# Kernel tuning notes

Measured on AMD Instinct MI355X. Metric: run time of the kernel, lower is better.

Reference implementation:

```python
import jax, jax.numpy as jnp
import numpy as np

CX, CY, FX, FY = 334.081, 169.808, 460.585, 460.268
EPS = 1e-07
T_ITER = 1000
MIN_POINTS = 5000
H, W, B = 360, 640, 2


def _point_cloud(depth_img):
    # depth_img: [C,H,W]; channel 2 if C==3 else channel 0
    depth = depth_img[2] if depth_img.shape[0] == 3 else depth_img[0]
    rows, cols = depth.shape
    c = jnp.arange(cols, dtype=depth.dtype)[None, :]
    r = jnp.arange(rows, dtype=depth.dtype)[:, None]
    valid = (depth > 0) & (depth < 65535)
    nanv = jnp.float32(jnp.nan)
    z = jnp.where(valid, depth / 1000.0, nanv)
    x = jnp.where(valid, z * (c - CX) / FX, nanv)
    y = jnp.where(valid, z * (r - CY) / FY, nanv)
    pcd = jnp.stack([x.ravel(), y.ravel(), z.ravel()], axis=1)  # [N,3]
    return pcd, valid.ravel()


def setup_inputs() -> dict:
    key = jax.random.key(0)
    k1, k2 = jax.random.split(key)
    fake = jax.random.uniform(k1, (B, 1, H, W), dtype=jnp.float32)
    real = jax.random.uniform(k2, (B, 1, H, W), dtype=jnp.float32)
    return {"fake": fake, "real": real, "epoch": 5, "show_image": 0}


def _forward(fake, real, epoch):
    real_pcd, vr = _point_cloud(real[0])
    fake_pcd, vf = _point_cloud(fake[0])
    real_pcd = real_pcd * 1000.0
    fake_pcd = fake_pcd * 1000.0
    # pcd[pcd==0] = eps  (NaN==0 is False, NaNs preserved)
    real_pcd = jnp.where(real_pcd == 0, EPS, real_pcd)
    fake_pcd = jnp.where(fake_pcd == 0, EPS, fake_pcd)

    # combined validity mask (real-valid then fake-valid filtering chain)
    m = vr & vf
    cnt = jnp.maximum(jnp.sum(m), 1)

    def sel(v, fill):
        return jnp.where(m, v, fill)

    def mrmse(a, b):
        d = sel(a, 0.0) - sel(b, 0.0)
        return jnp.sqrt(jnp.sum(d * d) / cnt)

    lossX = mrmse(real_pcd[:, 0], fake_pcd[:, 0])
    lossY = mrmse(real_pcd[:, 1], fake_pcd[:, 1])
    lossZ = mrmse(real_pcd[:, 2], fake_pcd[:, 2])
    dlog = jnp.log(jnp.abs(sel(real_pcd[:, 2], 1.0))) - jnp.log(jnp.abs(sel(fake_pcd[:, 2], 1.0)))
    RMSE_log = 10000.0 * jnp.sqrt(jnp.sum(jnp.where(m, dlog * dlog, 0.0)) / cnt)
    loss17 = RMSE_log * jnp.abs(10.0 * (3.0 - jnp.exp(lossX) - jnp.exp(lossY) - jnp.exp(lossZ)))

    # ---- batched RANSAC plane fit on normalized fake cloud ----
    nan_cloud = jnp.where(jnp.isnan(fake_pcd), 0.0, fake_pcd)
    pts = nan_cloud / jnp.max(nan_cloud)  # [N,3]
    N = pts.shape[0]
    thresh = jnp.maximum(jnp.float32(0.025 - 0.001 * epoch), jnp.float32(0.005))

    rkey = jax.random.key(42)
    idx = jax.random.randint(rkey, (T_ITER, 3), 0, N)  # 3 sample points per trial
    p = pts[idx]  # [T,3,3]
    vA = p[:, 1] - p[:, 0]
    vB = p[:, 2] - p[:, 0]
    nrm = jnp.cross(vA, vB)
    nrm = nrm / jnp.linalg.norm(nrm, axis=1, keepdims=True)  # unit normals [T,3]
    kk = -jnp.sum(nrm * p[:, 1], axis=1)  # plane offsets [T]
    dist = pts @ nrm.T + kk[None, :]  # [N,T], |n|=1 so no extra divide
    inl = jnp.abs(dist) <= thresh  # [N,T]
    counts = jnp.sum(inl, axis=0)  # [T]
    # keep first trial with strictly-largest count among counts > minPoints
    score = jnp.where(counts > MIN_POINTS, counts, -1)
    best = jnp.argmax(score)
    a, b, c, d = nrm[best, 0], nrm[best, 1], nrm[best, 2], kk[best]
    inlier_mask = inl[:, best]  # [N]

    # translation/rotation were built via torch.tensor(...) -> detached in torch
    trans = jax.lax.stop_gradient(jnp.stack([jnp.zeros(()), jnp.zeros(()), d / c]))
    n2 = a * a + b * b + c * c
    cos_t = c / jnp.sqrt(n2)
    sin_t = jnp.sqrt((a * a + b * b) / n2)
    sab = jnp.sqrt(a * a + b * b)
    u1 = b / sab
    u2 = -a / sab
    R = jnp.stack([
        jnp.stack([cos_t + u1 * u1 * (1 - cos_t), u1 * u2 * (1 - cos_t), u2 * sin_t]),
        jnp.stack([u1 * u2 * (1 - cos_t), cos_t + u2 * u2 * (1 - cos_t), -u1 * sin_t]),
        jnp.stack([-u2 * sin_t, u1 * sin_t, cos_t]),
    ])
    Rt = jax.lax.stop_gradient(R).T  # torch transposes before matmul

    plane_pts = pts + trans
    zc = (plane_pts @ Rt)[:, 2]  # rotated z for all points; inliers selected by mask
    icnt = jnp.maximum(jnp.sum(inlier_mask), 1)
    zmax = jnp.max(jnp.where(inlier_mask, zc, -jnp.inf))
    zmin = jnp.min(jnp.where(inlier_mask, zc, jnp.inf))
    below = jnp.sum(jnp.where(inlier_mask, jnp.abs(zc - zmax), 0.0)) / icnt
    above = jnp.sum(jnp.where(inlier_mask, jnp.abs(zc - zmin), 0.0)) / icnt
    above = jnp.where(above == 0, jnp.float32(1e-07), above)
    plane_mean_dist_grad = 1000.0 * (above + below)

    loss_curv = loss17 + plane_mean_dist_grad
    delta = jnp.stack([RMSE_log, lossX, lossY, lossZ, plane_mean_dist_grad, loss17])
    return delta, loss_curv


def reference(fake, real, epoch, show_image):
    del show_image  # unused in the loss math
    return _forward(fake, real, epoch)
```

## Files before the change

### kernel.cpp

```cpp
#include <hip/hip_runtime.h>

namespace {

typedef float v2f __attribute__((ext_vector_type(2)));

constexpr int kW = 640;
constexpr int kN = 230400;
constexpr unsigned kSpan = 230400u;
constexpr int kB1 = 900;
constexpr int kB3 = 1024;
constexpr int kPPB3 = 225;
constexpr int kB5 = 900;
constexpr unsigned kPoison = 0xAAAAAAAAu;

struct __align__(16) Acc {
  double lossX, lossY, lossZ, rmse_log, loss17;
  float maxv;
  unsigned selkey;
};

constexpr size_t kOffAcc     = 0;
constexpr size_t kOffC1      = 256;
constexpr size_t kOffC3      = 320;
constexpr size_t kOffC5      = 384;
constexpr size_t kOffPlanes  = 512;
constexpr size_t kOffSP      = 512 + 16384;
constexpr size_t kOffZP      = kOffSP + 43200;
constexpr size_t kOffPartial = kOffZP + 28800;
constexpr size_t kOffPts     = kOffPartial + (size_t)kB3 * 256 * 4;

__device__ __forceinline__ void ast64(unsigned long long* p, unsigned long long v) {
  __hip_atomic_store(p, v, __ATOMIC_RELAXED, __HIP_MEMORY_SCOPE_AGENT);
}
__device__ __forceinline__ unsigned long long ald64(const unsigned long long* p) {
  return __hip_atomic_load(p, __ATOMIC_RELAXED, __HIP_MEMORY_SCOPE_AGENT);
}
__device__ __forceinline__ void ast32(unsigned* p, unsigned v) {
  __hip_atomic_store(p, v, __ATOMIC_RELAXED, __HIP_MEMORY_SCOPE_AGENT);
}
__device__ __forceinline__ unsigned ald32(const unsigned* p) {
  return __hip_atomic_load(p, __ATOMIC_RELAXED, __HIP_MEMORY_SCOPE_AGENT);
}

__device__ __forceinline__ unsigned rotl32(unsigned v, int r) {
  return (v << r) | (v >> (32 - r));
}

__device__ __forceinline__ void threefry(unsigned c0, unsigned c1,
                                         unsigned& o0, unsigned& o1) {
  const unsigned ks0 = 0u, ks1 = 42u, ks2 = 0x1BD11BDAu ^ 0u ^ 42u;
  unsigned x0 = c0 + ks0, x1 = c1 + ks1;
#define TFR(r) { x0 += x1; x1 = rotl32(x1, (r)); x1 ^= x0; }
  TFR(13) TFR(15) TFR(26) TFR(6)
  x0 += ks1; x1 += ks2 + 1u;
  TFR(17) TFR(29) TFR(16) TFR(24)
  x0 += ks2; x1 += ks0 + 2u;
  TFR(13) TFR(15) TFR(26) TFR(6)
  x0 += ks0; x1 += ks1 + 3u;
  TFR(17) TFR(29) TFR(16) TFR(24)
  x0 += ks1; x1 += ks2 + 4u;
  TFR(13) TFR(15) TFR(26) TFR(6)
  x0 += ks2; x1 += ks0 + 5u;
#undef TFR
  o0 = x0; o1 = x1;
}

__device__ __forceinline__ void pix_coords(float d, int row, int col, bool& valid,
                                           float& x, float& y, float& z) {
  valid = (d > 0.0f) && (d < 65535.0f);
  float z0 = d / 1000.0f;
  float x0 = z0 * ((float)col - 334.081f) / 460.585f;
  float y0 = z0 * ((float)row - 169.808f) / 460.268f;
  x = x0 * 1000.0f;
  y = y0 * 1000.0f;
  z = z0 * 1000.0f;
  if (x == 0.0f) x = 1e-7f;
  if (y == 0.0f) y = 1e-7f;
  if (z == 0.0f) z = 1e-7f;
}

__device__ __forceinline__ void make_pt(float d, int row, int col, float maxv,
                                        float& x, float& y, float& z) {
  bool v; float a, b, c;
  pix_coords(d, row, col, v, a, b, c);
  x = (v ? a : 0.f) / maxv;
  y = (v ? b : 0.f) / maxv;
  z = (v ? c : 0.f) / maxv;
}

__device__ __forceinline__ float get_thresh(int ep) {
  return (float)fmax(0.025 - 0.001 * (double)ep, 0.005);
}

__global__ __launch_bounds__(256) void k_stats(const float* __restrict__ fake,
                                               const float* __restrict__ real,
                                               float* __restrict__ out,
                                               char* __restrict__ ws) {
  Acc* acc = (Acc*)(ws + kOffAcc);
  unsigned* ctr = (unsigned*)(ws + kOffC1);
  float4* planes = (float4*)(ws + kOffPlanes);
  unsigned long long* sp = (unsigned long long*)(ws + kOffSP);
  float4* ptsraw = (float4*)(ws + kOffPts);

  const int b = blockIdx.x, t = threadIdx.x;
  const int lane = t & 63, wid = t >> 6;

  __shared__ double sD0[4], sD1[4], sD2[4], sD3[4];
  __shared__ int sI0[4];
  __shared__ float sF0[4];
  __shared__ unsigned sArr;
  __shared__ float sMaxv;

  {
    int i = b * 256 + t;
    int row = i / kW, col = i - row * kW;
    bool vr, vf; float rx, ry, rz, fx, fy, fz;
    pix_coords(real[i], row, col, vr, rx, ry, rz);
    pix_coords(fake[i], row, col, vf, fx, fy, fz);
    ptsraw[i] = make_float4(vf ? fx : 0.f, vf ? fy : 0.f, vf ? fz : 0.f, 0.f);
    double dx2 = 0, dy2 = 0, dz2 = 0, dl2 = 0; int cc = 0;
    if (vr && vf) {
      float ddx = rx - fx, ddy = ry - fy, ddz = rz - fz;
      dx2 = (double)ddx * (double)ddx;
      dy2 = (double)ddy * (double)ddy;
      dz2 = (double)ddz * (double)ddz;
      double dl = log(fabs((double)rz)) - log(fabs((double)fz));
      dl2 = dl * dl;
      cc = 1;
    }
    float mx = vf ? fmaxf(fmaxf(fx, fy), fz) : 0.0f;
    for (int o = 32; o; o >>= 1) {
      dx2 += __shfl_down(dx2, o); dy2 += __shfl_down(dy2, o);
      dz2 += __shfl_down(dz2, o); dl2 += __shfl_down(dl2, o);
      cc += __shfl_down(cc, o);
      mx = fmaxf(mx, __shfl_down(mx, o));
    }
    if (lane == 0) { sD0[wid]=dx2; sD1[wid]=dy2; sD2[wid]=dz2; sD3[wid]=dl2;
                     sI0[wid]=cc; sF0[wid]=mx; }
    __syncthreads();
    if (t == 0) {
      unsigned long long* e = sp + (size_t)b * 6;
      ast64(e + 0, __double_as_longlong(sD0[0]+sD0[1]+sD0[2]+sD0[3]));
      ast64(e + 1, __double_as_longlong(sD1[0]+sD1[1]+sD1[2]+sD1[3]));
      ast64(e + 2, __double_as_longlong(sD2[0]+sD2[1]+sD2[2]+sD2[3]));
      ast64(e + 3, __double_as_longlong(sD3[0]+sD3[1]+sD3[2]+sD3[3]));
      ast64(e + 4, (unsigned long long)(sI0[0]+sI0[1]+sI0[2]+sI0[3]));
      float bm = fmaxf(fmaxf(sF0[0], sF0[1]), fmaxf(sF0[2], sF0[3]));
      ast64(e + 5, (unsigned long long)__float_as_uint(bm));
    }
  }
  __syncthreads();
  if (t == 0)
    sArr = __hip_atomic_fetch_add(ctr, 1u, __ATOMIC_RELAXED, __HIP_MEMORY_SCOPE_AGENT);
  __syncthreads();
  if (sArr != kPoison + (unsigned)(kB1 - 1)) return;

  {
    double gx = 0, gy = 0, gz = 0, gl = 0; int gc = 0; float gm = 0.f;
    for (int r = t; r < kB1; r += 256) {
      const unsigned long long* e = sp + (size_t)r * 6;
      gx += __longlong_as_double(ald64(e + 0));
      gy += __longlong_as_double(ald64(e + 1));
      gz += __longlong_as_double(ald64(e + 2));
      gl += __longlong_as_double(ald64(e + 3));
      gc += (int)ald64(e + 4);
      gm = fmaxf(gm, __uint_as_float((unsigned)ald64(e + 5)));
    }
    for (int o = 32; o; o >>= 1) {
      gx += __shfl_down(gx, o); gy += __shfl_down(gy, o);
      gz += __shfl_down(gz, o); gl += __shfl_down(gl, o);
      gc += __shfl_down(gc, o);
      gm = fmaxf(gm, __shfl_down(gm, o));
    }
    if (lane == 0) { sD0[wid]=gx; sD1[wid]=gy; sD2[wid]=gz; sD3[wid]=gl;
                     sI0[wid]=gc; sF0[wid]=gm; }
    __syncthreads();
    if (t == 0) {
      double SX = sD0[0]+sD0[1]+sD0[2]+sD0[3];
      double SY = sD1[0]+sD1[1]+sD1[2]+sD1[3];
      double SZ = sD2[0]+sD2[1]+sD2[2]+sD2[3];
      double SL = sD3[0]+sD3[1]+sD3[2]+sD3[3];
      int CN = sI0[0]+sI0[1]+sI0[2]+sI0[3];
      float MX = fmaxf(fmaxf(sF0[0], sF0[1]), fmaxf(sF0[2], sF0[3]));
      double cntd = (CN > 0) ? (double)CN : 1.0;
      double lossX = sqrt(SX / cntd);
      double lossY = sqrt(SY / cntd);
      double lossZ = sqrt(SZ / cntd);
      double rmse_log = 10000.0 * sqrt(SL / cntd);
      double loss17 = rmse_log * fabs(10.0 * (3.0 - exp(lossX) - exp(lossY) - exp(lossZ)));
      acc->lossX = lossX; acc->lossY = lossY; acc->lossZ = lossZ;
      acc->rmse_log = rmse_log; acc->loss17 = loss17;
      acc->maxv = MX;
      acc->selkey = 0u;
      out[0] = (float)rmse_log;
      out[1] = (float)lossX;
      out[2] = (float)lossY;
      out[3] = (float)lossZ;
      out[5] = (float)loss17;
      sMaxv = MX;
    }
    __syncthreads();
  }
  {
    float maxv = sMaxv;
#pragma unroll
    for (int j = 0; j < 4; j++) {
      int pid = t * 4 + j;
      if (pid < 1000) {
        float px[3], py[3], pz[3];
#pragma unroll
        for (int v = 0; v < 3; v++) {
          unsigned p = 3u * (unsigned)pid + (unsigned)v;
          unsigned o0, o1;
          threefry(p, p + 3000u, o0, o1);
          unsigned idx = o1 % kSpan;
          int row = (int)(idx / kW), col = (int)idx - row * kW;
          make_pt(fake[idx], row, col, maxv, px[v], py[v], pz[v]);
        }
        float ax = px[1]-px[0], ay = py[1]-py[0], az = pz[1]-pz[0];
        float bx = px[2]-px[0], by = py[2]-py[0], bz = pz[2]-pz[0];
        float nx = ay*bz - az*by;
        float ny = az*bx - ax*bz;
        float nz = ax*by - ay*bx;
        float nn = sqrtf(nx*nx + ny*ny + nz*nz);
        nx /= nn; ny /= nn; nz /= nn;
        float kk = -(nx*px[1] + ny*py[1] + nz*pz[1]);
        planes[pid] = make_float4(nx, ny, nz, kk);
      } else {
        planes[pid] = make_float4(0.f, 0.f, 0.f, 3e38f);
      }
    }
  }
}

__global__ __launch_bounds__(256) void k_count(const int* __restrict__ epoch,
                                               char* __restrict__ ws) {
  Acc* acc = (Acc*)(ws + kOffAcc);
  unsigned* ctr = (unsigned*)(ws + kOffC3);
  const float4* planes = (const float4*)(ws + kOffPlanes);
  unsigned* partial = (unsigned*)(ws + kOffPartial);
  const float4* ptsraw = (const float4*)(ws + kOffPts);

  const int b = blockIdx.x, t = threadIdx.x;
  const float th = get_thresh(*epoch);
  const float maxv = acc->maxv;

  __shared__ float4 sPts[kPPB3];
  __shared__ uint4 sAcc[16][16];
  __shared__ unsigned sArr;

  if (t < kPPB3) {
    float4 r = ptsraw[b * kPPB3 + t];
    sPts[t] = make_float4(r.x / maxv, r.y / maxv, r.z / maxv, 0.f);
  }
  float4 p0 = planes[t * 4 + 0], p1 = planes[t * 4 + 1];
  float4 p2 = planes[t * 4 + 2], p3 = planes[t * 4 + 3];
  v2f Ax = {p0.x, p1.x}, Ay = {p0.y, p1.y}, Az = {p0.z, p1.z}, Aw = {p0.w, p1.w};
  v2f Bx = {p2.x, p3.x}, By = {p2.y, p3.y}, Bz = {p2.z, p3.z}, Bw = {p2.w, p3.w};
  __syncthreads();

  int c0 = 0, c1 = 0, c2 = 0, c3 = 0;
#pragma unroll 5
  for (int s = 0; s < kPPB3; ++s) {
    float4 q = sPts[s];
    v2f qx = {q.x, q.x}, qy = {q.y, q.y}, qz = {q.z, q.z};
    v2f dA = __builtin_elementwise_fma(qx, Ax,
             __builtin_elementwise_fma(qy, Ay,
             __builtin_elementwise_fma(qz, Az, Aw)));
    v2f dB = __builtin_elementwise_fma(qx, Bx,
             __builtin_elementwise_fma(qy, By,
             __builtin_elementwise_fma(qz, Bz, Bw)));
    c0 += (fabsf(dA.x) <= th) ? 1 : 0;
    c1 += (fabsf(dA.y) <= th) ? 1 : 0;
    c2 += (fabsf(dB.x) <= th) ? 1 : 0;
    c3 += (fabsf(dB.y) <= th) ? 1 : 0;
  }
  ast32(&partial[b * 256 + t],
        (unsigned)c0 | ((unsigned)c1 << 8) | ((unsigned)c2 << 16) | ((unsigned)c3 << 24));

  __syncthreads();
  if (t == 0)
    sArr = __hip_atomic_fetch_add(ctr, 1u, __ATOMIC_RELAXED, __HIP_MEMORY_SCOPE_AGENT);
  __syncthreads();
  unsigned ret = sArr;
  if (ret < kPoison + (unsigned)(kB3 - 16)) return;

  int r = (int)(ret - (kPoison + (unsigned)(kB3 - 16)));
  if (t == 0) {
    while (ald32(ctr) != kPoison + (unsigned)kB3) __builtin_amdgcn_s_sleep(2);
  }
  __syncthreads();

  int owner = r * 16 + (t & 15);
  int chunk = t >> 4;
  unsigned s0 = 0, s1 = 0, s2 = 0, s3 = 0;
  for (int row = chunk * 64; row < chunk * 64 + 64; ++row) {
    unsigned v = ald32(&partial[row * 256 + owner]);
    s0 += v & 0xFFu; s1 += (v >> 8) & 0xFFu;
    s2 += (v >> 16) & 0xFFu; s3 += (v >> 24) & 0xFFu;
  }
  sAcc[t & 15][chunk] = make_uint4(s0, s1, s2, s3);
  __syncthreads();

  unsigned mykey = 0u;
  if (t < 16) {
    unsigned t0 = 0, t1 = 0, t2 = 0, t3 = 0;
    for (int j = 0; j < 16; ++j) {
      uint4 v = sAcc[t][j];
      t0 += v.x; t1 += v.y; t2 += v.z; t3 += v.w;
    }
    unsigned tot[4] = {t0, t1, t2, t3};
    int pbase = (r * 16 + t) * 4;
#pragma unroll
    for (int k = 0; k < 4; ++k) {
      int p = pbase + k;
      if (p < 1000) {
        int score = ((int)tot[k] > 5000) ? (int)tot[k] : -1;
        unsigned key = ((unsigned)(score + 2) << 10) | (unsigned)(1023 - p);
        mykey = key > mykey ? key : mykey;
      }
    }
  }
  for (int o = 32; o; o >>= 1) {
    unsigned other = __shfl_down(mykey, o);
    mykey = other > mykey ? other : mykey;
  }
  if (t == 0) atomicMax(&acc->selkey, mykey);
}

__global__ __launch_bounds__(256) void k_zc(const int* __restrict__ epoch,
                                            float* __restrict__ out,
                                            char* __restrict__ ws) {
  Acc* acc = (Acc*)(ws + kOffAcc);
  unsigned* ctr = (unsigned*)(ws + kOffC5);
  const float4* planes = (const float4*)(ws + kOffPlanes);
  unsigned long long* zp = (unsigned long long*)(ws + kOffZP);
  const float4* ptsraw = (const float4*)(ws + kOffPts);

  const int b = blockIdx.x, t = threadIdx.x;
  const int lane = t & 63, wid = t >> 6;
  const float th = get_thresh(*epoch);
  const float maxv = acc->maxv;

  int best = 1023 - (int)(acc->selkey & 1023u);
  float4 pl = planes[best];
  const float a = pl.x, bb = pl.y, c = pl.z, d = pl.w;
  float n2 = a * a + bb * bb + c * c;
  float cos_t = c / sqrtf(n2);
  float sin_t = sqrtf((a * a + bb * bb) / n2);
  float sab = sqrtf(a * a + bb * bb);
  float u1 = bb / sab, u2 = -a / sab;
  const float r0 = -u2 * sin_t, r1 = u1 * sin_t, r2 = cos_t, tz = d / c;

  __shared__ double sD0[4];
  __shared__ int sI0[4];
  __shared__ float sF0[4], sF1[4];
  __shared__ unsigned sArr;

  double sz = 0.0; int ic = 0; float zmx = -INFINITY, zmn = -INFINITY;
  {
    float4 rw = ptsraw[b * 256 + t];
    float qx = rw.x / maxv, qy = rw.y / maxv, qz = rw.z / maxv;
    float dist = fmaf(qx, a, fmaf(qy, bb, fmaf(qz, c, d)));
    if (fabsf(dist) <= th) {
      float zc = fmaf(qx, r0, fmaf(qy, r1, (qz + tz) * r2));
      sz = (double)zc; ic = 1; zmx = zc; zmn = -zc;
    }
  }
  for (int o = 32; o; o >>= 1) {
    sz += __shfl_down(sz, o); ic += __shfl_down(ic, o);
    zmx = fmaxf(zmx, __shfl_down(zmx, o));
    zmn = fmaxf(zmn, __shfl_down(zmn, o));
  }
  if (lane == 0) { sD0[wid] = sz; sI0[wid] = ic; sF0[wid] = zmx; sF1[wid] = zmn; }
  __syncthreads();
  if (t == 0) {
    unsigned long long* e = zp + (size_t)b * 4;
    ast64(e + 0, __double_as_longlong(sD0[0]+sD0[1]+sD0[2]+sD0[3]));
    ast64(e + 1, (unsigned long long)(sI0[0]+sI0[1]+sI0[2]+sI0[3]));
    float bmx = fmaxf(fmaxf(sF0[0], sF0[1]), fmaxf(sF0[2], sF0[3]));
    float bmn = fmaxf(fmaxf(sF1[0], sF1[1]), fmaxf(sF1[2], sF1[3]));
    ast64(e + 2, (unsigned long long)__float_as_uint(bmx) |
                 ((unsigned long long)__float_as_uint(bmn) << 32));
  }
  __syncthreads();
  if (t == 0)
    sArr = __hip_atomic_fetch_add(ctr, 1u, __ATOMIC_RELAXED, __HIP_MEMORY_SCOPE_AGENT);
  __syncthreads();
  if (sArr != kPoison + (unsigned)(kB5 - 1)) return;

  {
    double gs = 0.0; int gi = 0; float gmx = -INFINITY, gmn = -INFINITY;
    for (int r = t; r < kB5; r += 256) {
      const unsigned long long* e = zp + (size_t)r * 4;
      gs += __longlong_as_double(ald64(e + 0));
      gi += (int)ald64(e + 1);
      unsigned long long mm = ald64(e + 2);
      gmx = fmaxf(gmx, __uint_as_float((unsigned)(mm & 0xFFFFFFFFu)));
      gmn = fmaxf(gmn, __uint_as_float((unsigned)(mm >> 32)));
    }
    for (int o = 32; o; o >>= 1) {
      gs += __shfl_down(gs, o); gi += __shfl_down(gi, o);
      gmx = fmaxf(gmx, __shfl_down(gmx, o));
      gmn = fmaxf(gmn, __shfl_down(gmn, o));
    }
    if (lane == 0) { sD0[wid] = gs; sI0[wid] = gi; sF0[wid] = gmx; sF1[wid] = gmn; }
    __syncthreads();
    if (t == 0) {
      double S = sD0[0]+sD0[1]+sD0[2]+sD0[3];
      int IC = sI0[0]+sI0[1]+sI0[2]+sI0[3];
      float MX = fmaxf(fmaxf(sF0[0], sF0[1]), fmaxf(sF0[2], sF0[3]));
      float MN = fmaxf(fmaxf(sF1[0], sF1[1]), fmaxf(sF1[2], sF1[3]));
      double below = 0.0, above = 0.0;
      if (IC > 0) {
        double icd = (double)IC;
        double mean = S / icd;
        below = (double)MX - mean;
        above = mean - (double)(-MN);
      }
      if (above == 0.0) above = 1e-7;
      double pmdg = 1000.0 * (above + below);
      out[4] = (float)pmdg;
      out[6] = (float)(acc->loss17 + pmdg);
    }
  }
}

}

extern "C" void kernel_launch(void* const* d_in, const int* in_sizes, int n_in,
                              void* d_out, int out_size, void* d_ws, size_t ws_size,
                              hipStream_t stream) {
  (void)in_sizes; (void)n_in; (void)out_size; (void)ws_size;
  const float* fake = (const float*)d_in[0];
  const float* real = (const float*)d_in[1];
  const int* epoch = (const int*)d_in[2];
  float* out = (float*)d_out;
  char* ws = (char*)d_ws;

  k_stats<<<kB1, 256, 0, stream>>>(fake, real, out, ws);
  k_count<<<kB3, 256, 0, stream>>>(epoch, ws);
  k_zc<<<kB5, 256, 0, stream>>>(epoch, out, ws);
}
```

Baseline: 136.9 us.

## Fuse plane scoring and inlier z-stats into one kernel, recompute points from input

```diff
diff --git a/kernel.cpp b/kernel.cpp
--- a/kernel.cpp
+++ b/kernel.cpp
@@ -5,29 +5,25 @@
 typedef float v2f __attribute__((ext_vector_type(2)));
 
 constexpr int kW = 640;
-constexpr int kN = 230400;
 constexpr unsigned kSpan = 230400u;
 constexpr int kB1 = 900;
-constexpr int kB3 = 1024;
-constexpr int kPPB3 = 225;
-constexpr int kB5 = 900;
+constexpr int kB2 = 512;
+constexpr int kPPB2 = 450;
+constexpr int kTail = 16;
+constexpr int kSlice = 230400 / kTail;
 constexpr unsigned kPoison = 0xAAAAAAAAu;
 
-struct __align__(16) Acc {
-  double lossX, lossY, lossZ, rmse_log, loss17;
-  float maxv;
-  unsigned selkey;
-};
-
-constexpr size_t kOffAcc     = 0;
-constexpr size_t kOffC1      = 256;
-constexpr size_t kOffC3      = 320;
-constexpr size_t kOffC5      = 384;
-constexpr size_t kOffPlanes  = 512;
-constexpr size_t kOffSP      = 512 + 16384;
-constexpr size_t kOffZP      = kOffSP + 43200;
-constexpr size_t kOffPartial = kOffZP + 28800;
-constexpr size_t kOffPts     = kOffPartial + (size_t)kB3 * 256 * 4;
+constexpr size_t kOffMaxv   = 0;
+constexpr size_t kOffL17    = 8;
+constexpr size_t kOffSel    = 16;
+constexpr size_t kOffC1     = 128;
+constexpr size_t kOffC2     = 192;
+constexpr size_t kOffC2b    = 256;
+constexpr size_t kOffC3     = 320;
+constexpr size_t kOffPlanes = 512;
+constexpr size_t kOffSP     = 17408;
+constexpr size_t kOffZP     = 60928;
+constexpr size_t kOffPart   = 65536;
 
 __device__ __forceinline__ void ast64(unsigned long long* p, unsigned long long v) {
   __hip_atomic_store(p, v, __ATOMIC_RELAXED, __HIP_MEMORY_SCOPE_AGENT);
@@ -96,11 +92,12 @@
                                                const float* __restrict__ real,
                                                float* __restrict__ out,
                                                char* __restrict__ ws) {
-  Acc* acc = (Acc*)(ws + kOffAcc);
+  unsigned long long* wMaxv = (unsigned long long*)(ws + kOffMaxv);
+  unsigned long long* wL17 = (unsigned long long*)(ws + kOffL17);
+  unsigned* wSel = (unsigned*)(ws + kOffSel);
   unsigned* ctr = (unsigned*)(ws + kOffC1);
   float4* planes = (float4*)(ws + kOffPlanes);
   unsigned long long* sp = (unsigned long long*)(ws + kOffSP);
-  float4* ptsraw = (float4*)(ws + kOffPts);
 
   const int b = blockIdx.x, t = threadIdx.x;
   const int lane = t & 63, wid = t >> 6;
@@ -117,7 +114,6 @@
     bool vr, vf; float rx, ry, rz, fx, fy, fz;
     pix_coords(real[i], row, col, vr, rx, ry, rz);
     pix_coords(fake[i], row, col, vf, fx, fy, fz);
-    ptsraw[i] = make_float4(vf ? fx : 0.f, vf ? fy : 0.f, vf ? fz : 0.f, 0.f);
     double dx2 = 0, dy2 = 0, dz2 = 0, dl2 = 0; int cc = 0;
     if (vr && vf) {
       float ddx = rx - fx, ddy = ry - fy, ddz = rz - fz;
@@ -151,7 +147,7 @@
   }
   __syncthreads();
   if (t == 0)
-    sArr = __hip_atomic_fetch_add(ctr, 1u, __ATOMIC_RELAXED, __HIP_MEMORY_SCOPE_AGENT);
+    sArr = __hip_atomic_fetch_add(ctr, 1u, __ATOMIC_ACQ_REL, __HIP_MEMORY_SCOPE_AGENT);
   __syncthreads();
   if (sArr != kPoison + (unsigned)(kB1 - 1)) return;
 
@@ -188,15 +184,14 @@
       double lossZ = sqrt(SZ / cntd);
       double rmse_log = 10000.0 * sqrt(SL / cntd);
       double loss17 = rmse_log * fabs(10.0 * (3.0 - exp(lossX) - exp(lossY) - exp(lossZ)));
-      acc->lossX = lossX; acc->lossY = lossY; acc->lossZ = lossZ;
-      acc->rmse_log = rmse_log; acc->loss17 = loss17;
-      acc->maxv = MX;
-      acc->selkey = 0u;
       out[0] = (float)rmse_log;
       out[1] = (float)lossX;
       out[2] = (float)lossY;
       out[3] = (float)lossZ;
       out[5] = (float)loss17;
+      ast64(wMaxv, (unsigned long long)__float_as_uint(MX));
+      ast64(wL17, __double_as_longlong(loss17));
+      ast32(wSel, 0u);
       sMaxv = MX;
     }
     __syncthreads();
@@ -206,6 +201,7 @@
 #pragma unroll
     for (int j = 0; j < 4; j++) {
       int pid = t * 4 + j;
+      float4 pl;
       if (pid < 1000) {
         float px[3], py[3], pz[3];
 #pragma unroll
@@ -225,33 +221,53 @@
         float nn = sqrtf(nx*nx + ny*ny + nz*nz);
         nx /= nn; ny /= nn; nz /= nn;
         float kk = -(nx*px[1] + ny*py[1] + nz*pz[1]);
-        planes[pid] = make_float4(nx, ny, nz, kk);
+        pl = make_float4(nx, ny, nz, kk);
       } else {
-        planes[pid] = make_float4(0.f, 0.f, 0.f, 3e38f);
+        pl = make_float4(0.f, 0.f, 0.f, 3e38f);
       }
-    }
-  }
-}
-
-__global__ __launch_bounds__(256) void k_count(const int* __restrict__ epoch,
+      planes[pid] = pl;
+    }
+  }
+}
+
+__global__ __launch_bounds__(256) void k_count(const float* __restrict__ fake,
+                                               const int* __restrict__ epoch,
+                                               float* __restrict__ out,
                                                char* __restrict__ ws) {
-  Acc* acc = (Acc*)(ws + kOffAcc);
-  unsigned* ctr = (unsigned*)(ws + kOffC3);
+  const unsigned long long* wMaxv = (const unsigned long long*)(ws + kOffMaxv);
+  const unsigned long long* wL17 = (const unsigned long long*)(ws + kOffL17);
+  unsigned* wSel = (unsigned*)(ws + kOffSel);
+  unsigned* wC2 = (unsigned*)(ws + kOffC2);
+  unsigned* wC2b = (unsigned*)(ws + kOffC2b);
+  unsigned* wC3 = (unsigned*)(ws + kOffC3);
   const float4* planes = (const float4*)(ws + kOffPlanes);
-  unsigned* partial = (unsigned*)(ws + kOffPartial);
-  const float4* ptsraw = (const float4*)(ws + kOffPts);
+  unsigned long long* zp = (unsigned long long*)(ws + kOffZP);
+  unsigned long long* part = (unsigned long long*)(ws + kOffPart);
 
   const int b = blockIdx.x, t = threadIdx.x;
+  const int lane = t & 63, wid = t >> 6;
   const float th = get_thresh(*epoch);
-  const float maxv = acc->maxv;
-
-  __shared__ float4 sPts[kPPB3];
+  const float maxv = __uint_as_float((unsigned)*wMaxv);
+
+  __shared__ float4 sPts[kPPB2];
   __shared__ uint4 sAcc[16][16];
+  __shared__ double sD0[4];
+  __shared__ int sI0[4];
+  __shared__ float sF0[4], sF1[4];
   __shared__ unsigned sArr;
 
-  if (t < kPPB3) {
-    float4 r = ptsraw[b * kPPB3 + t];
-    sPts[t] = make_float4(r.x / maxv, r.y / maxv, r.z / maxv, 0.f);
+  {
+    int i = b * kPPB2 + t;
+    int row = i / kW, col = i - row * kW;
+    float x, y, z;
+    make_pt(fake[i], row, col, maxv, x, y, z);
+    sPts[t] = make_float4(x, y, z, 0.f);
+    if (t < kPPB2 - 256) {
+      int i2 = i + 256;
+      int row2 = i2 / kW, col2 = i2 - row2 * kW;
+      make_pt(fake[i2], row2, col2, maxv, x, y, z);
+      sPts[t + 256] = make_float4(x, y, z, 0.f);
+    }
   }
   float4 p0 = planes[t * 4 + 0], p1 = planes[t * 4 + 1];
   float4 p2 = planes[t * 4 + 2], p3 = planes[t * 4 + 3];
@@ -259,9 +275,9 @@
   v2f Bx = {p2.x, p3.x}, By = {p2.y, p3.y}, Bz = {p2.z, p3.z}, Bw = {p2.w, p3.w};
   __syncthreads();
 
-  int c0 = 0, c1 = 0, c2 = 0, c3 = 0;
-#pragma unroll 5
-  for (int s = 0; s < kPPB3; ++s) {
+  unsigned c0 = 0, c1 = 0, c2 = 0, c3 = 0;
+#pragma unroll 6
+  for (int s = 0; s < kPPB2; ++s) {
     float4 q = sPts[s];
     v2f qx = {q.x, q.x}, qy = {q.y, q.y}, qz = {q.z, q.z};
     v2f dA = __builtin_elementwise_fma(qx, Ax,
@@ -270,158 +286,151 @@
     v2f dB = __builtin_elementwise_fma(qx, Bx,
              __builtin_elementwise_fma(qy, By,
              __builtin_elementwise_fma(qz, Bz, Bw)));
-    c0 += (fabsf(dA.x) <= th) ? 1 : 0;
-    c1 += (fabsf(dA.y) <= th) ? 1 : 0;
-    c2 += (fabsf(dB.x) <= th) ? 1 : 0;
-    c3 += (fabsf(dB.y) <= th) ? 1 : 0;
-  }
-  ast32(&partial[b * 256 + t],
-        (unsigned)c0 | ((unsigned)c1 << 8) | ((unsigned)c2 << 16) | ((unsigned)c3 << 24));
-
+    c0 += (fabsf(dA.x) <= th) ? 1u : 0u;
+    c1 += (fabsf(dA.y) <= th) ? 1u : 0u;
+    c2 += (fabsf(dB.x) <= th) ? 1u : 0u;
+    c3 += (fabsf(dB.y) <= th) ? 1u : 0u;
+  }
+  ast64(&part[(size_t)b * 256 + t],
+        ((unsigned long long)(c0 | (c1 << 16))) |
+        ((unsigned long long)(c2 | (c3 << 16)) << 32));
   __syncthreads();
   if (t == 0)
-    sArr = __hip_atomic_fetch_add(ctr, 1u, __ATOMIC_RELAXED, __HIP_MEMORY_SCOPE_AGENT);
+    sArr = __hip_atomic_fetch_add(wC2, 1u, __ATOMIC_ACQ_REL, __HIP_MEMORY_SCOPE_AGENT);
   __syncthreads();
   unsigned ret = sArr;
-  if (ret < kPoison + (unsigned)(kB3 - 16)) return;
-
-  int r = (int)(ret - (kPoison + (unsigned)(kB3 - 16)));
+  if (ret < kPoison + (unsigned)(kB2 - kTail)) return;
+  const int r = (int)(ret - (kPoison + (unsigned)(kB2 - kTail)));
+
   if (t == 0) {
-    while (ald32(ctr) != kPoison + (unsigned)kB3) __builtin_amdgcn_s_sleep(2);
-  }
-  __syncthreads();
-
-  int owner = r * 16 + (t & 15);
-  int chunk = t >> 4;
-  unsigned s0 = 0, s1 = 0, s2 = 0, s3 = 0;
-  for (int row = chunk * 64; row < chunk * 64 + 64; ++row) {
-    unsigned v = ald32(&partial[row * 256 + owner]);
-    s0 += v & 0xFFu; s1 += (v >> 8) & 0xFFu;
-    s2 += (v >> 16) & 0xFFu; s3 += (v >> 24) & 0xFFu;
-  }
-  sAcc[t & 15][chunk] = make_uint4(s0, s1, s2, s3);
-  __syncthreads();
-
-  unsigned mykey = 0u;
-  if (t < 16) {
-    unsigned t0 = 0, t1 = 0, t2 = 0, t3 = 0;
-    for (int j = 0; j < 16; ++j) {
-      uint4 v = sAcc[t][j];
-      t0 += v.x; t1 += v.y; t2 += v.z; t3 += v.w;
-    }
-    unsigned tot[4] = {t0, t1, t2, t3};
-    int pbase = (r * 16 + t) * 4;
+    while (__hip_atomic_load(wC2, __ATOMIC_ACQUIRE, __HIP_MEMORY_SCOPE_AGENT)
+           != kPoison + (unsigned)kB2)
+      __builtin_amdgcn_s_sleep(2);
+  }
+  __syncthreads();
+  {
+    int owner = r * 16 + (t & 15);
+    int chunk = t >> 4;
+    unsigned s0 = 0, s1 = 0, s2 = 0, s3 = 0;
+    for (int row = chunk * 32; row < chunk * 32 + 32; ++row) {
+      unsigned long long v = ald64(&part[(size_t)row * 256 + owner]);
+      s0 += (unsigned)(v & 0xFFFFu);
+      s1 += (unsigned)((v >> 16) & 0xFFFFu);
+      s2 += (unsigned)((v >> 32) & 0xFFFFu);
+      s3 += (unsigned)(v >> 48);
+    }
+    sAcc[t & 15][chunk] = make_uint4(s0, s1, s2, s3);
+  }
+  __syncthreads();
+  {
+    unsigned mykey = 0u;
+    if (t < 16) {
+      unsigned t0 = 0, t1 = 0, t2 = 0, t3 = 0;
+      for (int j = 0; j < 16; ++j) {
+        uint4 v = sAcc[t][j];
+        t0 += v.x; t1 += v.y; t2 += v.z; t3 += v.w;
+      }
+      unsigned tot[4] = {t0, t1, t2, t3};
+      int pbase = (r * 16 + t) * 4;
 #pragma unroll
-    for (int k = 0; k < 4; ++k) {
-      int p = pbase + k;
-      if (p < 1000) {
+      for (int k = 0; k < 4; ++k) {
+        int p = pbase + k;
         int score = ((int)tot[k] > 5000) ? (int)tot[k] : -1;
         unsigned key = ((unsigned)(score + 2) << 10) | (unsigned)(1023 - p);
         mykey = key > mykey ? key : mykey;
       }
     }
-  }
-  for (int o = 32; o; o >>= 1) {
-    unsigned other = __shfl_down(mykey, o);
-    mykey = other > mykey ? other : mykey;
-  }
-  if (t == 0) atomicMax(&acc->selkey, mykey);
-}
-
-__global__ __launch_bounds__(256) void k_zc(const int* __restrict__ epoch,
-                                            float* __restrict__ out,
-                                            char* __restrict__ ws) {
-  Acc* acc = (Acc*)(ws + kOffAcc);
-  unsigned* ctr = (unsigned*)(ws + kOffC5);
-  const float4* planes = (const float4*)(ws + kOffPlanes);
-  unsigned long long* zp = (unsigned long long*)(ws + kOffZP);
-  const float4* ptsraw = (const float4*)(ws + kOffPts);
-
-  const int b = blockIdx.x, t = threadIdx.x;
-  const int lane = t & 63, wid = t >> 6;
-  const float th = get_thresh(*epoch);
-  const float maxv = acc->maxv;
-
-  int best = 1023 - (int)(acc->selkey & 1023u);
-  float4 pl = planes[best];
-  const float a = pl.x, bb = pl.y, c = pl.z, d = pl.w;
-  float n2 = a * a + bb * bb + c * c;
-  float cos_t = c / sqrtf(n2);
-  float sin_t = sqrtf((a * a + bb * bb) / n2);
-  float sab = sqrtf(a * a + bb * bb);
-  float u1 = bb / sab, u2 = -a / sab;
-  const float r0 = -u2 * sin_t, r1 = u1 * sin_t, r2 = cos_t, tz = d / c;
-
-  __shared__ double sD0[4];
-  __shared__ int sI0[4];
-  __shared__ float sF0[4], sF1[4];
-  __shared__ unsigned sArr;
-
-  double sz = 0.0; int ic = 0; float zmx = -INFINITY, zmn = -INFINITY;
-  {
-    float4 rw = ptsraw[b * 256 + t];
-    float qx = rw.x / maxv, qy = rw.y / maxv, qz = rw.z / maxv;
-    float dist = fmaf(qx, a, fmaf(qy, bb, fmaf(qz, c, d)));
-    if (fabsf(dist) <= th) {
-      float zc = fmaf(qx, r0, fmaf(qy, r1, (qz + tz) * r2));
-      sz = (double)zc; ic = 1; zmx = zc; zmn = -zc;
-    }
-  }
-  for (int o = 32; o; o >>= 1) {
-    sz += __shfl_down(sz, o); ic += __shfl_down(ic, o);
-    zmx = fmaxf(zmx, __shfl_down(zmx, o));
-    zmn = fmaxf(zmn, __shfl_down(zmn, o));
-  }
-  if (lane == 0) { sD0[wid] = sz; sI0[wid] = ic; sF0[wid] = zmx; sF1[wid] = zmn; }
-  __syncthreads();
-  if (t == 0) {
-    unsigned long long* e = zp + (size_t)b * 4;
-    ast64(e + 0, __double_as_longlong(sD0[0]+sD0[1]+sD0[2]+sD0[3]));
-    ast64(e + 1, (unsigned long long)(sI0[0]+sI0[1]+sI0[2]+sI0[3]));
-    float bmx = fmaxf(fmaxf(sF0[0], sF0[1]), fmaxf(sF0[2], sF0[3]));
-    float bmn = fmaxf(fmaxf(sF1[0], sF1[1]), fmaxf(sF1[2], sF1[3]));
-    ast64(e + 2, (unsigned long long)__float_as_uint(bmx) |
-                 ((unsigned long long)__float_as_uint(bmn) << 32));
-  }
-  __syncthreads();
-  if (t == 0)
-    sArr = __hip_atomic_fetch_add(ctr, 1u, __ATOMIC_RELAXED, __HIP_MEMORY_SCOPE_AGENT);
-  __syncthreads();
-  if (sArr != kPoison + (unsigned)(kB5 - 1)) return;
-
-  {
+    for (int o = 32; o; o >>= 1) {
+      unsigned other = __shfl_down(mykey, o);
+      mykey = other > mykey ? other : mykey;
+    }
+    if (t == 0) {
+      atomicMax(wSel, mykey);
+      __hip_atomic_fetch_add(wC2b, 1u, __ATOMIC_RELEASE, __HIP_MEMORY_SCOPE_AGENT);
+      while (__hip_atomic_load(wC2b, __ATOMIC_ACQUIRE, __HIP_MEMORY_SCOPE_AGENT)
+             != kPoison + (unsigned)kTail)
+        __builtin_amdgcn_s_sleep(2);
+      sArr = __hip_atomic_load(wSel, __ATOMIC_RELAXED, __HIP_MEMORY_SCOPE_AGENT);
+    }
+  }
+  __syncthreads();
+
+  {
+    int best = 1023 - (int)(sArr & 1023u);
+    float4 pl = planes[best];
+    const float a = pl.x, bb = pl.y, c = pl.z, d = pl.w;
+    float n2 = a * a + bb * bb + c * c;
+    float cos_t = c / sqrtf(n2);
+    float sin_t = sqrtf((a * a + bb * bb) / n2);
+    float sab = sqrtf(a * a + bb * bb);
+    float u1 = bb / sab, u2 = -a / sab;
+    const float r0 = -u2 * sin_t, r1 = u1 * sin_t, r2 = cos_t, tz = d / c;
+
+    double sz = 0.0; int ic = 0; float zmx = -INFINITY, zmn = -INFINITY;
+    for (int k = t; k < kSlice; k += 256) {
+      int i = r * kSlice + k;
+      int row = i / kW, col = i - row * kW;
+      float qx, qy, qz;
+      make_pt(fake[i], row, col, maxv, qx, qy, qz);
+      float dist = fmaf(qx, a, fmaf(qy, bb, fmaf(qz, c, d)));
+      if (fabsf(dist) <= th) {
+        float zc = fmaf(qx, r0, fmaf(qy, r1, (qz + tz) * r2));
+        sz += (double)zc; ic++;
+        zmx = fmaxf(zmx, zc);
+        zmn = fmaxf(zmn, -zc);
+      }
+    }
+    for (int o = 32; o; o >>= 1) {
+      sz += __shfl_down(sz, o); ic += __shfl_down(ic, o);
+      zmx = fmaxf(zmx, __shfl_down(zmx, o));
+      zmn = fmaxf(zmn, __shfl_down(zmn, o));
+    }
+    if (lane == 0) { sD0[wid] = sz; sI0[wid] = ic; sF0[wid] = zmx; sF1[wid] = zmn; }
+    __syncthreads();
+    if (t == 0) {
+      unsigned long long* e = zp + (size_t)r * 4;
+      ast64(e + 0, __double_as_longlong(sD0[0]+sD0[1]+sD0[2]+sD0[3]));
+      ast64(e + 1, (unsigned long long)(sI0[0]+sI0[1]+sI0[2]+sI0[3]));
+      float bmx = fmaxf(fmaxf(sF0[0], sF0[1]), fmaxf(sF0[2], sF0[3]));
+      float bmn = fmaxf(fmaxf(sF1[0], sF1[1]), fmaxf(sF1[2], sF1[3]));
+      ast64(e + 2, (unsigned long long)__float_as_uint(bmx) |
+                   ((unsigned long long)__float_as_uint(bmn) << 32));
+    }
+    __syncthreads();
+    if (t == 0)
+      sArr = __hip_atomic_fetch_add(wC3, 1u, __ATOMIC_ACQ_REL, __HIP_MEMORY_SCOPE_AGENT);
+    __syncthreads();
+    if (sArr != kPoison + (unsigned)(kTail - 1)) return;
+  }
+
+  if (t < 64) {
     double gs = 0.0; int gi = 0; float gmx = -INFINITY, gmn = -INFINITY;
-    for (int r = t; r < kB5; r += 256) {
-      const unsigned long long* e = zp + (size_t)r * 4;
-      gs += __longlong_as_double(ald64(e + 0));
-      gi += (int)ald64(e + 1);
+    if (t < kTail) {
+      const unsigned long long* e = zp + (size_t)t * 4;
+      gs = __longlong_as_double(ald64(e + 0));
+      gi = (int)ald64(e + 1);
       unsigned long long mm = ald64(e + 2);
-      gmx = fmaxf(gmx, __uint_as_float((unsigned)(mm & 0xFFFFFFFFu)));
-      gmn = fmaxf(gmn, __uint_as_float((unsigned)(mm >> 32)));
-    }
-    for (int o = 32; o; o >>= 1) {
+      gmx = __uint_as_float((unsigned)(mm & 0xFFFFFFFFu));
+      gmn = __uint_as_float((unsigned)(mm >> 32));
+    }
+    for (int o = 8; o; o >>= 1) {
       gs += __shfl_down(gs, o); gi += __shfl_down(gi, o);
       gmx = fmaxf(gmx, __shfl_down(gmx, o));
       gmn = fmaxf(gmn, __shfl_down(gmn, o));
     }
-    if (lane == 0) { sD0[wid] = gs; sI0[wid] = gi; sF0[wid] = gmx; sF1[wid] = gmn; }
-    __syncthreads();
     if (t == 0) {
-      double S = sD0[0]+sD0[1]+sD0[2]+sD0[3];
-      int IC = sI0[0]+sI0[1]+sI0[2]+sI0[3];
-      float MX = fmaxf(fmaxf(sF0[0], sF0[1]), fmaxf(sF0[2], sF0[3]));
-      float MN = fmaxf(fmaxf(sF1[0], sF1[1]), fmaxf(sF1[2], sF1[3]));
       double below = 0.0, above = 0.0;
-      if (IC > 0) {
-        double icd = (double)IC;
-        double mean = S / icd;
-        below = (double)MX - mean;
-        above = mean - (double)(-MN);
+      if (gi > 0) {
+        double icd = (double)gi;
+        double mean = gs / icd;
+        below = (double)gmx - mean;
+        above = mean - (double)(-gmn);
       }
       if (above == 0.0) above = 1e-7;
       double pmdg = 1000.0 * (above + below);
+      double loss17 = __longlong_as_double(*wL17);
       out[4] = (float)pmdg;
-      out[6] = (float)(acc->loss17 + pmdg);
+      out[6] = (float)(loss17 + pmdg);
     }
   }
 }
@@ -439,6 +448,5 @@
   char* ws = (char*)d_ws;
 
   k_stats<<<kB1, 256, 0, stream>>>(fake, real, out, ws);
-  k_count<<<kB3, 256, 0, stream>>>(epoch, ws);
-  k_zc<<<kB5, 256, 0, stream>>>(epoch, out, ws);
-}
+  k_count<<<kB2, 256, 0, stream>>>(fake, epoch, out, ws);
+}
```

Result: slower. 156.1 us (+14.0%).
